# Kernel optimization log

Measured on AMD Instinct MI355X. Metric: run time of the kernel, lower is better.

The kernel has to match this reference:

```python
import jax, jax.numpy as jnp
import numpy as np
import math

B, S, D, H = 4, 2048, 1024, 16
DK = D // H
DFF = 1024  # FeedForward default d_ff=1024 (DecoderLayer passes only d_model)
EPS = 1e-6
SQRT_2_OVER_PI = math.sqrt(2.0 / math.pi)


def setup_inputs() -> dict:
    key = jax.random.key(0)
    ks = jax.random.split(key, 12)
    sc = 0.02
    x = jax.random.normal(ks[0], (B, S, D), dtype=jnp.float32)
    # causal look-ahead mask: 1 where attendable, 0 where masked
    mask = jnp.broadcast_to(jnp.tril(jnp.ones((S, S), dtype=jnp.int32)), (B, S, S))
    inp = {
        'x': x,
        'mask': mask,
        'Wq': jax.random.normal(ks[1], (D, D), jnp.float32) * sc,
        'bq': jnp.zeros((D,), jnp.float32),
        'Wk': jax.random.normal(ks[2], (D, D), jnp.float32) * sc,
        'bk': jnp.zeros((D,), jnp.float32),
        'Wv': jax.random.normal(ks[3], (D, D), jnp.float32) * sc,
        'bv': jnp.zeros((D,), jnp.float32),
        'Wo': jax.random.normal(ks[4], (D, D), jnp.float32) * sc,
        'bo': jnp.zeros((D,), jnp.float32),
        'W1': jax.random.normal(ks[5], (D, DFF), jnp.float32) * sc,
        'b1': jnp.zeros((DFF,), jnp.float32),
        'W2': jax.random.normal(ks[6], (DFF, D), jnp.float32) * sc,
        'b2': jnp.zeros((D,), jnp.float32),
        'alpha1': jnp.ones((D,), jnp.float32),
        'bias1': jnp.zeros((D,), jnp.float32),
        'alpha2': jnp.ones((D,), jnp.float32),
        'bias2': jnp.zeros((D,), jnp.float32),
    }
    return inp


def _norm(x, alpha, bias):
    # torch: (x - mean) / (x.std(unbiased=True) + eps) * alpha + bias
    mean = jnp.mean(x, axis=-1, keepdims=True)
    var = jnp.sum((x - mean) ** 2, axis=-1, keepdims=True) / (x.shape[-1] - 1)
    std = jnp.sqrt(var)
    return alpha * (x - mean) / (std + EPS) + bias


def _gelu(x):
    return 0.5 * x * (1.0 + jnp.tanh(SQRT_2_OVER_PI * (x + 0.044715 * x ** 3)))


def reference(x, mask, Wq, bq, Wk, bk, Wv, bv, Wo, bo, W1, b1, W2, b2,
              alpha1, bias1, alpha2, bias2):
    b, s, d = x.shape
    x2 = _norm(x, alpha1, bias1)
    q = (x2 @ Wq + bq).reshape(b, s, H, DK).transpose(0, 2, 1, 3)  # bhsd
    k = (x2 @ Wk + bk).reshape(b, s, H, DK).transpose(0, 2, 1, 3)
    v = (x2 @ Wv + bv).reshape(b, s, H, DK).transpose(0, 2, 1, 3)
    scores = jnp.einsum('bhqd,bhkd->bhqk', q, k) / jnp.sqrt(jnp.float32(DK))
    scores = jnp.where(mask[:, None, :, :] == 0, jnp.float32(-1e9), scores)
    probs = jax.nn.softmax(scores, axis=-1)
    attn = jnp.einsum('bhqk,bhkd->bhqd', probs, v)
    concat = attn.transpose(0, 2, 1, 3).reshape(b, s, d)
    x = x + (concat @ Wo + bo)
    x2 = _norm(x, alpha2, bias2)
    ff = _gelu(x2 @ W1 + b1) @ W2 + b2
    return x + ff
```

## Files before the change

kernel.cpp:

```cpp
#include <hip/hip_runtime.h>
#include <hip/hip_bf16.h>
#include <math.h>


#define B_ 4
#define S_ 2048
#define D_ 1024
#define H_ 16
#define DFF_ 1024

typedef __attribute__((ext_vector_type(8))) short short8;
typedef __attribute__((ext_vector_type(8))) unsigned short ushort8;
typedef __attribute__((ext_vector_type(4))) float f32x4;

__device__ __forceinline__ unsigned short f2bf(float f) {
  __hip_bfloat16 h = __float2bfloat16(f);
  return *reinterpret_cast<unsigned short*>(&h);
}

__device__ __forceinline__ void gload16(const void* g, void* l) {
  __builtin_amdgcn_global_load_lds(
      (const __attribute__((address_space(1))) void*)g,
      (__attribute__((address_space(3))) void*)l, 16, 0, 0);
}

__global__ __launch_bounds__(256) void tcast6_k(
    const float* s0, const float* s1, const float* s2, const float* s3,
    const float* s4, const float* s5, unsigned short* d0, unsigned short* d1,
    unsigned short* d2, unsigned short* d3, unsigned short* d4,
    unsigned short* d5) {
  const float* src;
  unsigned short* dst;
  switch (blockIdx.z) {
    case 0: src = s0; dst = d0; break;
    case 1: src = s1; dst = d1; break;
    case 2: src = s2; dst = d2; break;
    case 3: src = s3; dst = d3; break;
    case 4: src = s4; dst = d4; break;
    default: src = s5; dst = d5; break;
  }
  __shared__ float tile[64][65];
  const int k0 = blockIdx.y * 64, n0 = blockIdx.x * 64;
  const int t = threadIdx.x;
  const int r = t >> 2, c0 = (t & 3) * 16;
  const float4* sp =
      reinterpret_cast<const float4*>(src + (size_t)(k0 + r) * 1024 + n0 + c0);
#pragma unroll
  for (int j = 0; j < 4; ++j) {
    float4 v = sp[j];
    tile[r][c0 + 4 * j] = v.x;
    tile[r][c0 + 4 * j + 1] = v.y;
    tile[r][c0 + 4 * j + 2] = v.z;
    tile[r][c0 + 4 * j + 3] = v.w;
  }
  __syncthreads();
  ushort8 o0, o1;
#pragma unroll
  for (int j = 0; j < 8; ++j) o0[j] = f2bf(tile[c0 + j][r]);
#pragma unroll
  for (int j = 0; j < 8; ++j) o1[j] = f2bf(tile[c0 + 8 + j][r]);
  unsigned short* dp = dst + (size_t)(n0 + r) * 1024 + k0 + c0;
  *reinterpret_cast<ushort8*>(dp) = o0;
  *reinterpret_cast<ushort8*>(dp + 8) = o1;
}

__global__ __launch_bounds__(256) void ln_k(const float* __restrict__ x,
                                            const float* __restrict__ alpha,
                                            const float* __restrict__ bias,
                                            unsigned short* __restrict__ out) {
  int row = blockIdx.x, t = threadIdx.x;
  float4 v = reinterpret_cast<const float4*>(x + (size_t)row * D_)[t];
  float s = v.x + v.y + v.z + v.w;
  float q = v.x * v.x + v.y * v.y + v.z * v.z + v.w * v.w;
#pragma unroll
  for (int off = 32; off > 0; off >>= 1) {
    s += __shfl_down(s, off);
    q += __shfl_down(q, off);
  }
  __shared__ float ss[4], sq[4], stat[2];
  if ((t & 63) == 0) { ss[t >> 6] = s; sq[t >> 6] = q; }
  __syncthreads();
  if (t == 0) {
    float S = ss[0] + ss[1] + ss[2] + ss[3];
    float Q = sq[0] + sq[1] + sq[2] + sq[3];
    float mean = S * (1.0f / D_);
    float var = fmaxf((Q - D_ * mean * mean) * (1.0f / (D_ - 1)), 0.0f);
    stat[0] = mean;
    stat[1] = 1.0f / (sqrtf(var) + 1e-6f);
  }
  __syncthreads();
  float mean = stat[0], inv = stat[1];
  float4 a = reinterpret_cast<const float4*>(alpha)[t];
  float4 b = reinterpret_cast<const float4*>(bias)[t];
  ushort4 o;
  o.x = f2bf((v.x - mean) * inv * a.x + b.x);
  o.y = f2bf((v.y - mean) * inv * a.y + b.y);
  o.z = f2bf((v.z - mean) * inv * a.z + b.z);
  o.w = f2bf((v.w - mean) * inv * a.w + b.w);
  reinterpret_cast<ushort4*>(out + (size_t)row * D_)[t] = o;
}

__device__ __forceinline__ void gemm_core64(
    const unsigned short* __restrict__ A, const unsigned short* __restrict__ Wt,
    int m0, int n0, int K, unsigned short* As ,
    unsigned short* Bs , f32x4 (&acc)[2][4]) {
  const int t = threadIdx.x;
  const int wv = t >> 6, lane = t & 63, quad = lane >> 4, l16 = lane & 15;
  const int wm = wv >> 1, wn = wv & 1;
  const int lr8 = lane >> 3;
  const int lseg = ((lane & 7) ^ lr8) * 8;

  const unsigned short* Ag0 = A + (size_t)(m0 + wv * 16 + lr8) * K + lseg;
  const unsigned short* Ag1 = A + (size_t)(m0 + wv * 16 + 8 + lr8) * K + lseg;
  const unsigned short* Bg0 = Wt + (size_t)(n0 + wv * 32 + lr8) * K + lseg;
  const unsigned short* Bg1 = Wt + (size_t)(n0 + wv * 32 + 8 + lr8) * K + lseg;
  const unsigned short* Bg2 = Wt + (size_t)(n0 + wv * 32 + 16 + lr8) * K + lseg;
  const unsigned short* Bg3 = Wt + (size_t)(n0 + wv * 32 + 24 + lr8) * K + lseg;
  unsigned short* Al0 = &As[(wv * 16) * 64];
  unsigned short* Al1 = &As[(wv * 16 + 8) * 64];
  unsigned short* Bl0 = &Bs[(wv * 32) * 64];
  unsigned short* Bl1 = &Bs[(wv * 32 + 8) * 64];
  unsigned short* Bl2 = &Bs[(wv * 32 + 16) * 64];
  unsigned short* Bl3 = &Bs[(wv * 32 + 24) * 64];

  for (int k0 = 0; k0 < K; k0 += 64) {
    gload16(Ag0, Al0);
    gload16(Ag1, Al1);
    gload16(Bg0, Bl0);
    gload16(Bg1, Bl1);
    gload16(Bg2, Bl2);
    gload16(Bg3, Bl3);
    __syncthreads();
    short8 af[2][2], bf[2][4];
#pragma unroll
    for (int p = 0; p < 2; ++p) {
#pragma unroll
      for (int mt = 0; mt < 2; ++mt) {
        int r = wm * 32 + mt * 16 + l16;
        af[p][mt] = *reinterpret_cast<const short8*>(
            &As[r * 64 + (((p * 4 + quad) ^ (r & 7)) << 3)]);
      }
#pragma unroll
      for (int nt = 0; nt < 4; ++nt) {
        int r = wn * 64 + nt * 16 + l16;
        bf[p][nt] = *reinterpret_cast<const short8*>(
            &Bs[r * 64 + (((p * 4 + quad) ^ (r & 7)) << 3)]);
      }
    }
#pragma unroll
    for (int p = 0; p < 2; ++p)
#pragma unroll
      for (int mt = 0; mt < 2; ++mt)
#pragma unroll
        for (int nt = 0; nt < 4; ++nt)
          acc[mt][nt] = __builtin_amdgcn_mfma_f32_16x16x32_bf16(
              af[p][mt], bf[p][nt], acc[mt][nt], 0, 0, 0);
    __syncthreads();
    Ag0 += 64; Ag1 += 64; Bg0 += 64; Bg1 += 64; Bg2 += 64; Bg3 += 64;
  }
}

__global__ __launch_bounds__(256, 4) void gemm_k(
    const unsigned short* __restrict__ A, const unsigned short* __restrict__ Wt,
    const float* __restrict__ bias, const float* __restrict__ res,
    void* __restrict__ outp, int M, int N, int K, int flags) {
  __shared__ unsigned short As[64 * 64];
  __shared__ unsigned short Bs[128 * 64];
  const int t = threadIdx.x;
  const int m0 = blockIdx.y * 64, n0 = blockIdx.x * 128;
  const int wv = t >> 6, lane = t & 63, quad = lane >> 4, l16 = lane & 15;
  const int wm = wv >> 1, wn = wv & 1;
  f32x4 acc[2][4] = {};
  gemm_core64(A, Wt, m0, n0, K, As, Bs, acc);

  const bool obf = flags & 1, dog = flags & 2;
#pragma unroll
  for (int nt = 0; nt < 4; ++nt) {
    int col = n0 + wn * 64 + nt * 16 + l16;
    float bv = bias[col];
#pragma unroll
    for (int mt = 0; mt < 2; ++mt) {
#pragma unroll
      for (int r = 0; r < 4; ++r) {
        int row = m0 + wm * 32 + mt * 16 + quad * 4 + r;
        float v = acc[mt][nt][r] + bv;
        if (res) v += res[(size_t)row * N + col];
        if (dog) {
          float e = __expf(1.5957691216057308f * (v + 0.044715f * v * v * v));
          float th = 1.0f - 2.0f / (1.0f + e);
          v = 0.5f * v * (1.0f + th);
        }
        if (obf)
          ((unsigned short*)outp)[(size_t)row * N + col] = f2bf(v);
        else
          ((float*)outp)[(size_t)row * N + col] = v;
      }
    }
  }
}

__global__ __launch_bounds__(256, 4) void gemmqkv_k(
    const unsigned short* __restrict__ A, const unsigned short* __restrict__ Wt,
    const float* __restrict__ bq, const float* __restrict__ bk,
    const float* __restrict__ bv, unsigned short* __restrict__ outq,
    unsigned short* __restrict__ outk, unsigned short* __restrict__ outvt,
    int M, int K) {
  __shared__ unsigned short As[64 * 64];
  __shared__ unsigned short Bs[128 * 64];
  const int t = threadIdx.x;
  const int m0 = blockIdx.y * 64, n0 = blockIdx.x * 128;
  const int wv = t >> 6, lane = t & 63, quad = lane >> 4, l16 = lane & 15;
  const int wm = wv >> 1, wn = wv & 1;
  f32x4 acc[2][4] = {};
  gemm_core64(A, Wt, m0, n0, K, As, Bs, acc);

  const int seg = n0 >> 10;
  const int nb = n0 & 1023;
  const float* bias = (seg == 0) ? bq : (seg == 1) ? bk : bv;
  if (seg < 2) {
    unsigned short* o = (seg == 0) ? outq : outk;
#pragma unroll
    for (int nt = 0; nt < 4; ++nt) {
      int col = nb + wn * 64 + nt * 16 + l16;
      float bvv = bias[col];
#pragma unroll
      for (int mt = 0; mt < 2; ++mt)
#pragma unroll
        for (int r = 0; r < 4; ++r) {
          int row = m0 + wm * 32 + mt * 16 + quad * 4 + r;
          o[(size_t)row * D_ + col] = f2bf(acc[mt][nt][r] + bvv);
        }
    }
  } else {
#pragma unroll
    for (int nt = 0; nt < 4; ++nt) {
      int col = nb + wn * 64 + nt * 16 + l16;
      float bvv = bias[col];
      int h = col >> 6, dk = col & 63;
#pragma unroll
      for (int mt = 0; mt < 2; ++mt) {
        int m = m0 + wm * 32 + mt * 16 + quad * 4;
        int b = m >> 11, sidx = m & 2047;
        ushort4 o;
        o.x = f2bf(acc[mt][nt][0] + bvv);
        o.y = f2bf(acc[mt][nt][1] + bvv);
        o.z = f2bf(acc[mt][nt][2] + bvv);
        o.w = f2bf(acc[mt][nt][3] + bvv);
        *reinterpret_cast<ushort4*>(
            &outvt[(((size_t)(b * 16 + h) * 64 + dk) * 2048 + sidx)]) = o;
      }
    }
  }
}

__global__ __launch_bounds__(256, 2) void attn_k(
    const unsigned short* __restrict__ Q, const unsigned short* __restrict__ Kg,
    const unsigned short* __restrict__ VT, unsigned short* __restrict__ Og) {
  __shared__ unsigned short Ks[2][64 * 64];
  __shared__ unsigned short Vs[2][64 * 64];
  __shared__ unsigned short Ps[4 * 16 * 72];
  const int t = threadIdx.x;
  const int qt = 31 - (blockIdx.x >> 6);
  const int bh = blockIdx.x & 63;
  const int b = bh >> 4, h = bh & 15;
  const int w = t >> 6, lane = t & 63, quad = lane >> 4, l16 = lane & 15;
  const int q0 = qt * 64 + w * 16;
  unsigned short* PsW = &Ps[w * 16 * 72];

  short8 qf[2];
#pragma unroll
  for (int kc = 0; kc < 2; ++kc)
    qf[kc] = *reinterpret_cast<const short8*>(
        Q + (size_t)(b * S_ + q0 + l16) * D_ + h * 64 + kc * 32 + quad * 8);
  asm volatile("" ::"v"(qf[0]), "v"(qf[1]) : "memory");

  f32x4 Oh[4] = {};
  f32x4 sums = {};
  short8 onev;
#pragma unroll
  for (int j = 0; j < 8; ++j) onev[j] = (short)0x3F80;

  const int srA = w * 8 + (lane >> 3);
  const int ssA = ((lane & 7) ^ (srA & 7)) * 8;
  const int srB = srA + 32;
  const int ssB = ((lane & 7) ^ (srB & 7)) * 8;
  const unsigned short* KgA = Kg + (size_t)(b * S_ + srA) * D_ + h * 64 + ssA;
  const unsigned short* KgB = Kg + (size_t)(b * S_ + srB) * D_ + h * 64 + ssB;
  const unsigned short* VgA = VT + ((size_t)bh * 64 + srA) * 2048 + ssA;
  const unsigned short* VgB = VT + ((size_t)bh * 64 + srB) * 2048 + ssB;
  unsigned short* KlA = &Ks[0][(w * 8) * 64];
  unsigned short* KlB = &Ks[0][(32 + w * 8) * 64];
  unsigned short* VlA = &Vs[0][(w * 8) * 64];
  unsigned short* VlB = &Vs[0][(32 + w * 8) * 64];

  const float C0 = 0.18033688011f;
  const float C1 = -23.08312065f;

  gload16(KgA, KlA);
  gload16(KgB, KlB);
  gload16(VgA, VlA);
  gload16(VgB, VlB);
  KgA += (size_t)64 * D_;
  KgB += (size_t)64 * D_;
  VgA += 64;
  VgB += 64;

  for (int kt = 0; kt <= qt; ++kt) {
    const bool diag = (kt == qt);
    const int coff = (kt & 1) << 12;
    const int noff = ((kt & 1) ^ 1) << 12;

    if (kt < qt) {
      gload16(KgA, KlA + noff);
      gload16(KgB, KlB + noff);
      gload16(VgA, VlA + noff);
      gload16(VgB, VlB + noff);
      KgA += (size_t)64 * D_;
      KgB += (size_t)64 * D_;
      VgA += 64;
      VgB += 64;
      asm volatile("s_waitcnt vmcnt(4)" ::: "memory");
    } else {
      asm volatile("s_waitcnt vmcnt(0)" ::: "memory");
    }
    asm volatile("s_barrier" ::: "memory");

    const unsigned short* Ksc = &Ks[0][coff];
    const unsigned short* Vsc = &Vs[0][coff];

    f32x4 sch[4] = {};
#pragma unroll
    for (int mt = 0; mt < 4; ++mt) {
      int r = mt * 16 + l16;
      short8 kf0 = *reinterpret_cast<const short8*>(
          &Ksc[r * 64 + ((quad ^ (r & 7)) << 3)]);
      short8 kf1 = *reinterpret_cast<const short8*>(
          &Ksc[r * 64 + (((4 + quad) ^ (r & 7)) << 3)]);
      sch[mt] = __builtin_amdgcn_mfma_f32_16x16x32_bf16(kf0, qf[0], sch[mt],
                                                        0, 0, 0);
      sch[mt] = __builtin_amdgcn_mfma_f32_16x16x32_bf16(kf1, qf[1], sch[mt],
                                                        0, 0, 0);
    }

    {
      const int kb0 = kt * 64;
      const int q = q0 + l16;
#pragma unroll
      for (int mt = 0; mt < 4; ++mt) {
        float pv[4];
#pragma unroll
        for (int r = 0; r < 4; ++r) {
          int key = kb0 + mt * 16 + quad * 4 + r;
          float p = __builtin_amdgcn_exp2f(fmaf(sch[mt][r], C0, C1));
          if (diag && key > q) p = 0.0f;
          pv[r] = p;
        }
        ushort4 pk = {f2bf(pv[0]), f2bf(pv[1]), f2bf(pv[2]), f2bf(pv[3])};
        *reinterpret_cast<ushort4*>(&PsW[l16 * 72 + mt * 16 + quad * 4]) = pk;
      }
    }
    __builtin_amdgcn_sched_barrier(0);

    short8 pf[2];
#pragma unroll
    for (int kc = 0; kc < 2; ++kc)
      pf[kc] = *reinterpret_cast<const short8*>(
          &PsW[l16 * 72 + kc * 32 + quad * 8]);

#pragma unroll
    for (int kc = 0; kc < 2; ++kc) {
      sums = __builtin_amdgcn_mfma_f32_16x16x32_bf16(pf[kc], onev, sums,
                                                     0, 0, 0);
#pragma unroll
      for (int nd = 0; nd < 4; ++nd) {
        int r = nd * 16 + l16;
        short8 vf = *reinterpret_cast<const short8*>(
            &Vsc[r * 64 + (((kc * 4 + quad) ^ (r & 7)) << 3)]);
        Oh[nd] = __builtin_amdgcn_mfma_f32_16x16x32_bf16(pf[kc], vf, Oh[nd],
                                                         0, 0, 0);
      }
    }
    asm volatile("s_barrier" ::: "memory");
  }

#pragma unroll
  for (int r = 0; r < 4; ++r) {
    float rl = 1.0f / sums[r];
#pragma unroll
    for (int nd = 0; nd < 4; ++nd)
      Og[(size_t)(b * S_ + q0 + quad * 4 + r) * D_ + h * 64 + nd * 16 + l16] =
          f2bf(Oh[nd][r] * rl);
  }
}

extern "C" void kernel_launch(void* const* d_in, const int* in_sizes, int n_in,
                              void* d_out, int out_size, void* d_ws,
                              size_t ws_size, hipStream_t stream) {
  const float* x = (const float*)d_in[0];
  const float* Wq = (const float*)d_in[2];
  const float* bq = (const float*)d_in[3];
  const float* Wk = (const float*)d_in[4];
  const float* bk = (const float*)d_in[5];
  const float* Wv = (const float*)d_in[6];
  const float* bv = (const float*)d_in[7];
  const float* Wo = (const float*)d_in[8];
  const float* bo = (const float*)d_in[9];
  const float* W1 = (const float*)d_in[10];
  const float* b1 = (const float*)d_in[11];
  const float* W2 = (const float*)d_in[12];
  const float* b2 = (const float*)d_in[13];
  const float* alpha1 = (const float*)d_in[14];
  const float* bias1 = (const float*)d_in[15];
  const float* alpha2 = (const float*)d_in[16];
  const float* bias2 = (const float*)d_in[17];
  float* out = (float*)d_out;

  char* ws = (char*)d_ws;
  const size_t MB = 1024 * 1024;
  unsigned short* wqT = (unsigned short*)(ws + 0 * MB);
  unsigned short* wkT = (unsigned short*)(ws + 2 * MB);
  unsigned short* wvT = (unsigned short*)(ws + 4 * MB);
  unsigned short* woT = (unsigned short*)(ws + 6 * MB);
  unsigned short* w1T = (unsigned short*)(ws + 8 * MB);
  unsigned short* w2T = (unsigned short*)(ws + 10 * MB);
  unsigned short* x2a = (unsigned short*)(ws + 12 * MB);
  unsigned short* qb = (unsigned short*)(ws + 28 * MB);
  unsigned short* kb = (unsigned short*)(ws + 44 * MB);
  unsigned short* vtb = (unsigned short*)(ws + 60 * MB);

  tcast6_k<<<dim3(16, 16, 6), dim3(256), 0, stream>>>(Wq, Wk, Wv, Wo, W1, W2,
                                                      wqT, wkT, wvT, woT, w1T,
                                                      w2T);

  const int M = B_ * S_;
  ln_k<<<dim3(M), dim3(256), 0, stream>>>(x, alpha1, bias1, x2a);

  gemmqkv_k<<<dim3(24, 128), dim3(256), 0, stream>>>(x2a, wqT, bq, bk, bv, qb,
                                                     kb, vtb, M, D_);

  attn_k<<<dim3(2048), dim3(256), 0, stream>>>(qb, kb, vtb, x2a);

  dim3 gg(D_ / 128, M / 64);
  gemm_k<<<gg, dim3(256), 0, stream>>>(x2a, woT, bo, x, out, M, D_, D_, 0);

  ln_k<<<dim3(M), dim3(256), 0, stream>>>(out, alpha2, bias2, qb);

  gemm_k<<<gg, dim3(256), 0, stream>>>(qb, w1T, b1, nullptr, kb, M, DFF_, D_, 3);

  gemm_k<<<gg, dim3(256), 0, stream>>>(kb, w2T, b2, out, out, M, D_, DFF_, 0);
}
```

Measured before the change: 403.1 us.

## Enlarge GEMM tiles to 256x128 with double-buffered async LDS loads

Reworks the GEMM core so each block uses 512 threads on a 256x128 output tile, with each wave computing 64x64. Global-to-LDS loads are double-buffered through dynamic shared memory, and explicit vmcnt waits let the next K tile load while the current one is computed. The aim is more operand reuse per LDS tile, fewer barriers per FLOP, and hidden global-load latency. The costs are 96KB of LDS per block, fewer blocks in flight, more accumulator registers, and a smaller grid, which could hurt occupancy or tail balance.

```diff
diff --git a/kernel.cpp b/kernel.cpp
--- a/kernel.cpp
+++ b/kernel.cpp
@@ -100,78 +100,93 @@
   reinterpret_cast<ushort4*>(out + (size_t)row * D_)[t] = o;
 }
 
-__device__ __forceinline__ void gemm_core64(
+__device__ __forceinline__ void gemm_core256(
     const unsigned short* __restrict__ A, const unsigned short* __restrict__ Wt,
-    int m0, int n0, int K, unsigned short* As ,
-    unsigned short* Bs , f32x4 (&acc)[2][4]) {
+    int m0, int n0, int K, unsigned short* lds, f32x4 (&acc)[4][4]) {
   const int t = threadIdx.x;
   const int wv = t >> 6, lane = t & 63, quad = lane >> 4, l16 = lane & 15;
   const int wm = wv >> 1, wn = wv & 1;
-  const int lr8 = lane >> 3;
-  const int lseg = ((lane & 7) ^ lr8) * 8;
-
-  const unsigned short* Ag0 = A + (size_t)(m0 + wv * 16 + lr8) * K + lseg;
-  const unsigned short* Ag1 = A + (size_t)(m0 + wv * 16 + 8 + lr8) * K + lseg;
-  const unsigned short* Bg0 = Wt + (size_t)(n0 + wv * 32 + lr8) * K + lseg;
-  const unsigned short* Bg1 = Wt + (size_t)(n0 + wv * 32 + 8 + lr8) * K + lseg;
-  const unsigned short* Bg2 = Wt + (size_t)(n0 + wv * 32 + 16 + lr8) * K + lseg;
-  const unsigned short* Bg3 = Wt + (size_t)(n0 + wv * 32 + 24 + lr8) * K + lseg;
-  unsigned short* Al0 = &As[(wv * 16) * 64];
-  unsigned short* Al1 = &As[(wv * 16 + 8) * 64];
-  unsigned short* Bl0 = &Bs[(wv * 32) * 64];
-  unsigned short* Bl1 = &Bs[(wv * 32 + 8) * 64];
-  unsigned short* Bl2 = &Bs[(wv * 32 + 16) * 64];
-  unsigned short* Bl3 = &Bs[(wv * 32 + 24) * 64];
-
-  for (int k0 = 0; k0 < K; k0 += 64) {
-    gload16(Ag0, Al0);
-    gload16(Ag1, Al1);
-    gload16(Bg0, Bl0);
-    gload16(Bg1, Bl1);
-    gload16(Bg2, Bl2);
-    gload16(Bg3, Bl3);
-    __syncthreads();
-    short8 af[2][2], bf[2][4];
-#pragma unroll
-    for (int p = 0; p < 2; ++p) {
-#pragma unroll
-      for (int mt = 0; mt < 2; ++mt) {
-        int r = wm * 32 + mt * 16 + l16;
-        af[p][mt] = *reinterpret_cast<const short8*>(
-            &As[r * 64 + (((p * 4 + quad) ^ (r & 7)) << 3)]);
-      }
-#pragma unroll
-      for (int nt = 0; nt < 4; ++nt) {
-        int r = wn * 64 + nt * 16 + l16;
-        bf[p][nt] = *reinterpret_cast<const short8*>(
-            &Bs[r * 64 + (((p * 4 + quad) ^ (r & 7)) << 3)]);
-      }
-    }
-#pragma unroll
-    for (int p = 0; p < 2; ++p)
-#pragma unroll
-      for (int mt = 0; mt < 2; ++mt)
+  const int nt_tiles = K >> 6;
+
+  const unsigned short* gp[6];
+  int ub8[6];
+#pragma unroll
+  for (int g = 0; g < 6; ++g) {
+    int idx = g * 512 + t;
+    ub8[g] = (g * 512 + wv * 64) * 8;
+    if (idx < 2048) {
+      int row = idx >> 3, ps = idx & 7;
+      gp[g] = A + (size_t)(m0 + row) * K + (ps ^ (row & 7)) * 8;
+    } else {
+      int j = idx - 2048;
+      int row = j >> 3, ps = j & 7;
+      gp[g] = Wt + (size_t)(n0 + row) * K + (ps ^ (row & 7)) * 8;
+    }
+  }
+
+#define STAGE256(buf, kk)                                   \
+  {                                                         \
+    unsigned short* lb = lds + (buf)*24576;                 \
+    _Pragma("unroll") for (int g = 0; g < 6; ++g)           \
+        gload16(gp[g] + (kk), lb + ub8[g]);                 \
+  }
+
+  STAGE256(0, 0);
+  STAGE256(1, 64);
+
+  for (int kt = 0; kt < nt_tiles; ++kt) {
+    if (kt + 1 < nt_tiles)
+      asm volatile("s_waitcnt vmcnt(6)" ::: "memory");
+    else
+      asm volatile("s_waitcnt vmcnt(0)" ::: "memory");
+    asm volatile("s_barrier" ::: "memory");
+
+    const unsigned short* Ab = lds + (kt & 1) * 24576;
+    const unsigned short* Bb = Ab + 16384;
+
+    short8 af[4][2], bf[4][2];
+#pragma unroll
+    for (int mt = 0; mt < 4; ++mt) {
+      int r = wm * 64 + mt * 16 + l16;
+#pragma unroll
+      for (int kc = 0; kc < 2; ++kc)
+        af[mt][kc] = *reinterpret_cast<const short8*>(
+            &Ab[r * 64 + (((kc * 4 + quad) ^ (r & 7)) << 3)]);
+    }
+#pragma unroll
+    for (int nt = 0; nt < 4; ++nt) {
+      int r = wn * 64 + nt * 16 + l16;
+#pragma unroll
+      for (int kc = 0; kc < 2; ++kc)
+        bf[nt][kc] = *reinterpret_cast<const short8*>(
+            &Bb[r * 64 + (((kc * 4 + quad) ^ (r & 7)) << 3)]);
+    }
+#pragma unroll
+    for (int kc = 0; kc < 2; ++kc)
+#pragma unroll
+      for (int mt = 0; mt < 4; ++mt)
 #pragma unroll
         for (int nt = 0; nt < 4; ++nt)
           acc[mt][nt] = __builtin_amdgcn_mfma_f32_16x16x32_bf16(
-              af[p][mt], bf[p][nt], acc[mt][nt], 0, 0, 0);
-    __syncthreads();
-    Ag0 += 64; Ag1 += 64; Bg0 += 64; Bg1 += 64; Bg2 += 64; Bg3 += 64;
-  }
-}
-
-__global__ __launch_bounds__(256, 4) void gemm_k(
+              af[mt][kc], bf[nt][kc], acc[mt][nt], 0, 0, 0);
+
+    asm volatile("s_barrier" ::: "memory");
+    if (kt + 2 < nt_tiles) STAGE256(kt & 1, (kt + 2) << 6);
+  }
+#undef STAGE256
+}
+
+__global__ __launch_bounds__(512, 2) void gemm_k(
     const unsigned short* __restrict__ A, const unsigned short* __restrict__ Wt,
     const float* __restrict__ bias, const float* __restrict__ res,
     void* __restrict__ outp, int M, int N, int K, int flags) {
-  __shared__ unsigned short As[64 * 64];
-  __shared__ unsigned short Bs[128 * 64];
+  extern __shared__ unsigned short lds[];
   const int t = threadIdx.x;
-  const int m0 = blockIdx.y * 64, n0 = blockIdx.x * 128;
+  const int m0 = blockIdx.y * 256, n0 = blockIdx.x * 128;
   const int wv = t >> 6, lane = t & 63, quad = lane >> 4, l16 = lane & 15;
   const int wm = wv >> 1, wn = wv & 1;
-  f32x4 acc[2][4] = {};
-  gemm_core64(A, Wt, m0, n0, K, As, Bs, acc);
+  f32x4 acc[4][4] = {};
+  gemm_core256(A, Wt, m0, n0, K, lds, acc);
 
   const bool obf = flags & 1, dog = flags & 2;
 #pragma unroll
@@ -179,10 +194,10 @@
     int col = n0 + wn * 64 + nt * 16 + l16;
     float bv = bias[col];
 #pragma unroll
-    for (int mt = 0; mt < 2; ++mt) {
+    for (int mt = 0; mt < 4; ++mt) {
 #pragma unroll
       for (int r = 0; r < 4; ++r) {
-        int row = m0 + wm * 32 + mt * 16 + quad * 4 + r;
+        int row = m0 + wm * 64 + mt * 16 + quad * 4 + r;
         float v = acc[mt][nt][r] + bv;
         if (res) v += res[(size_t)row * N + col];
         if (dog) {
@@ -199,20 +214,19 @@
   }
 }
 
-__global__ __launch_bounds__(256, 4) void gemmqkv_k(
+__global__ __launch_bounds__(512, 2) void gemmqkv_k(
     const unsigned short* __restrict__ A, const unsigned short* __restrict__ Wt,
     const float* __restrict__ bq, const float* __restrict__ bk,
     const float* __restrict__ bv, unsigned short* __restrict__ outq,
     unsigned short* __restrict__ outk, unsigned short* __restrict__ outvt,
     int M, int K) {
-  __shared__ unsigned short As[64 * 64];
-  __shared__ unsigned short Bs[128 * 64];
+  extern __shared__ unsigned short lds[];
   const int t = threadIdx.x;
-  const int m0 = blockIdx.y * 64, n0 = blockIdx.x * 128;
+  const int m0 = blockIdx.y * 256, n0 = blockIdx.x * 128;
   const int wv = t >> 6, lane = t & 63, quad = lane >> 4, l16 = lane & 15;
   const int wm = wv >> 1, wn = wv & 1;
-  f32x4 acc[2][4] = {};
-  gemm_core64(A, Wt, m0, n0, K, As, Bs, acc);
+  f32x4 acc[4][4] = {};
+  gemm_core256(A, Wt, m0, n0, K, lds, acc);
 
   const int seg = n0 >> 10;
   const int nb = n0 & 1023;
@@ -224,10 +238,10 @@
       int col = nb + wn * 64 + nt * 16 + l16;
       float bvv = bias[col];
 #pragma unroll
-      for (int mt = 0; mt < 2; ++mt)
+      for (int mt = 0; mt < 4; ++mt)
 #pragma unroll
         for (int r = 0; r < 4; ++r) {
-          int row = m0 + wm * 32 + mt * 16 + quad * 4 + r;
+          int row = m0 + wm * 64 + mt * 16 + quad * 4 + r;
           o[(size_t)row * D_ + col] = f2bf(acc[mt][nt][r] + bvv);
         }
     }
@@ -238,8 +252,8 @@
       float bvv = bias[col];
       int h = col >> 6, dk = col & 63;
 #pragma unroll
-      for (int mt = 0; mt < 2; ++mt) {
-        int m = m0 + wm * 32 + mt * 16 + quad * 4;
+      for (int mt = 0; mt < 4; ++mt) {
+        int m = m0 + wm * 64 + mt * 16 + quad * 4;
         int b = m >> 11, sidx = m & 2047;
         ushort4 o;
         o.x = f2bf(acc[mt][nt][0] + bvv);
@@ -428,6 +442,17 @@
   unsigned short* kb = (unsigned short*)(ws + 44 * MB);
   unsigned short* vtb = (unsigned short*)(ws + 60 * MB);
 
+  static bool attr_set = false;
+  if (!attr_set) {
+    attr_set = true;
+    (void)hipFuncSetAttribute((const void*)gemm_k,
+                              hipFuncAttributeMaxDynamicSharedMemorySize,
+                              98304);
+    (void)hipFuncSetAttribute((const void*)gemmqkv_k,
+                              hipFuncAttributeMaxDynamicSharedMemorySize,
+                              98304);
+  }
+
   tcast6_k<<<dim3(16, 16, 6), dim3(256), 0, stream>>>(Wq, Wk, Wv, Wo, W1, W2,
                                                       wqT, wkT, wvT, woT, w1T,
                                                       w2T);
@@ -435,17 +460,19 @@
   const int M = B_ * S_;
   ln_k<<<dim3(M), dim3(256), 0, stream>>>(x, alpha1, bias1, x2a);
 
-  gemmqkv_k<<<dim3(24, 128), dim3(256), 0, stream>>>(x2a, wqT, bq, bk, bv, qb,
-                                                     kb, vtb, M, D_);
+  gemmqkv_k<<<dim3(24, 32), dim3(512), 98304, stream>>>(x2a, wqT, bq, bk, bv,
+                                                        qb, kb, vtb, M, D_);
 
   attn_k<<<dim3(2048), dim3(256), 0, stream>>>(qb, kb, vtb, x2a);
 
-  dim3 gg(D_ / 128, M / 64);
-  gemm_k<<<gg, dim3(256), 0, stream>>>(x2a, woT, bo, x, out, M, D_, D_, 0);
+  dim3 gg(D_ / 128, M / 256);
+  gemm_k<<<gg, dim3(512), 98304, stream>>>(x2a, woT, bo, x, out, M, D_, D_, 0);
 
   ln_k<<<dim3(M), dim3(256), 0, stream>>>(out, alpha2, bias2, qb);
 
-  gemm_k<<<gg, dim3(256), 0, stream>>>(qb, w1T, b1, nullptr, kb, M, DFF_, D_, 3);
-
-  gemm_k<<<gg, dim3(256), 0, stream>>>(kb, w2T, b2, out, out, M, D_, DFF_, 0);
-}
+  gemm_k<<<gg, dim3(512), 98304, stream>>>(qb, w1T, b1, nullptr, kb, M, DFF_,
+                                           D_, 3);
+
+  gemm_k<<<gg, dim3(512), 98304, stream>>>(kb, w2T, b2, out, out, M, D_, DFF_,
+                                           0);
+}
```

Result: no change. 409.2 us (+1.5%).
